# Performance work log

Hardware: AMD Instinct MI355X
Metric: run time of the kernel (lower is better)

## Reference

```python
import jax, jax.numpy as jnp
import numpy as np
import math
from jax import lax

F_SZ = 128      # feature_size
N_HEADS = 8
DH = F_SZ // N_HEADS
LANE_F = 64     # lane_feature_size
NUM_PREDS = 6
LEN_PRED = 30
B, V, T_PAST, N_LANES = 32, 64, 20, 128
SCALE = 1.0 / math.sqrt(DH)


def _heads(x):
    # [..., F] -> [..., H, dh]
    return x.reshape(*x.shape[:-1], N_HEADS, DH)


def _attn(q, k, v):
    # q: [..., H, Nq, dh], k/v: [..., H, Nk, dh] (broadcast over leading dims)
    s = jnp.einsum('...hqd,...hkd->...hqk', q, k) * SCALE
    p = jax.nn.softmax(s, axis=-1)
    return jnp.einsum('...hqk,...hkd->...hqd', p, v)


def _conv1(w, x):
    # 1x1 Conv2d (no bias): w [O,F], x [B,F,V,T]
    return jnp.einsum('of,bfvt->bovt', w, x)


def _to_tbhvd(x):
    # [B,F,V,T] -> [T,B,H,V,dh]  (matches permute(3,0,2,1).view(...).permute(0,1,3,2,4))
    return _heads(x.transpose(3, 0, 2, 1)).transpose(0, 1, 3, 2, 4)


def setup_inputs() -> dict:
    key = jax.random.key(0)
    ks = jax.random.split(key, 32)
    rn = lambda i, shp: jax.random.normal(ks[i], shp, dtype=jnp.float32)
    w = lambda i, shp: rn(i, shp) * 0.05
    return {
        'inputs': rn(0, (B, 2, V, T_PAST)),
        'lanes': rn(1, (B, N_LANES, LANE_F)),
        'pos': rn(2, (B, V, 2)),
        # Embedding conv (2 -> F, kernel (1,3), pad (0,1))
        'emb_w': w(3, (F_SZ, 2, 1, 3)), 'emb_b': w(4, (F_SZ,)),
        # LaneAttentionPast (Linear weights [out,in], no bias)
        'wq_past': w(5, (F_SZ, F_SZ)), 'wk_lanes_p': w(6, (F_SZ, LANE_F)),
        'wv_lanes_p': w(7, (F_SZ, LANE_F)), 'wc_past': w(8, (F_SZ, F_SZ)),
        # SelfAttentionFut (1x1 convs, no bias)
        'wk_fut': w(9, (F_SZ, F_SZ)), 'wq_fut_sa': w(10, (F_SZ, F_SZ)),
        'wv_fut': w(11, (F_SZ, F_SZ)), 'wc_fut_sa': w(12, (F_SZ, F_SZ)),
        # LaneAttentionFut
        'wk_lanes_f': w(13, (F_SZ, LANE_F)), 'wv_lanes_f': w(14, (F_SZ, LANE_F)),
        'wq_fut_la': w(15, (F_SZ, F_SZ)), 'wc_fut_la': w(16, (F_SZ, F_SZ)),
        # MultiOutputLayer (1x1 convs with bias)
        'w1': w(17, (F_SZ, F_SZ)), 'b1': w(18, (F_SZ,)),
        'w2': w(19, (F_SZ, F_SZ)), 'b2': w(20, (F_SZ,)),
        'wo': w(21, (6 * NUM_PREDS, F_SZ)), 'bo': w(22, (6 * NUM_PREDS,)),
    }


def reference(inputs, lanes, pos, emb_w, emb_b, wq_past, wk_lanes_p, wv_lanes_p,
              wc_past, wk_fut, wq_fut_sa, wv_fut, wc_fut_sa, wk_lanes_f,
              wv_lanes_f, wq_fut_la, wc_fut_la, w1, b1, w2, b2, wo, bo):
    # ---- Embedding: Conv2d(2->F, (1,3), pad (0,1)) over [B,2,V,T_past]
    emb = lax.conv_general_dilated(
        inputs, emb_w, (1, 1), ((0, 0), (1, 1)),
        dimension_numbers=('NCHW', 'OIHW', 'NCHW')) + emb_b[None, :, None, None]
    feat = emb[:, :, :, -1].transpose(0, 2, 1)            # [B,V,F] last timestep

    # ---- LaneAttentionPast: vehicles attend to lanes
    q = _heads(feat @ wq_past.T).transpose(0, 2, 1, 3)    # [B,H,V,dh]
    k = _heads(lanes @ wk_lanes_p.T).transpose(0, 2, 1, 3)  # [B,H,nl,dh]
    v = _heads(lanes @ wv_lanes_p.T).transpose(0, 2, 1, 3)
    o = _attn(q, k, v).transpose(0, 2, 1, 3).reshape(B, V, F_SZ)
    feat = o @ wc_past.T + feat                           # residual

    # ---- tile over prediction horizon: h [B,F,V,T]
    h = jnp.broadcast_to(feat.transpose(0, 2, 1)[:, :, :, None],
                         (B, F_SZ, V, LEN_PRED))

    # ---- SelfAttentionFut: per-timestep vehicle-vehicle attention
    k = _to_tbhvd(_conv1(wk_fut, h))                      # [T,B,H,V,dh]
    q = _to_tbhvd(_conv1(wq_fut_sa, h))
    vv = _to_tbhvd(_conv1(wv_fut, h))
    o = _attn(q, k, vv).transpose(0, 1, 3, 2, 4).reshape(LEN_PRED, B, V, F_SZ)
    h = _conv1(wc_fut_sa, o.transpose(1, 3, 2, 0)) + h    # residual

    # ---- LaneAttentionFut: per-timestep vehicle-lane attention
    kl = _heads(lanes @ wk_lanes_f.T).transpose(0, 2, 1, 3)[None]  # [1,B,H,nl,dh]
    vl = _heads(lanes @ wv_lanes_f.T).transpose(0, 2, 1, 3)[None]
    q = _to_tbhvd(_conv1(wq_fut_la, h))                   # [T,B,H,V,dh]
    o = _attn(q, kl, vl).transpose(0, 1, 3, 2, 4).reshape(LEN_PRED, B, V, F_SZ)
    h = _conv1(wc_fut_la, o.transpose(1, 3, 2, 0)) + h    # residual

    z = jax.nn.relu(_conv1(w1, h) + b1[None, :, None, None])
    z = jax.nn.relu(_conv1(w2, z) + b2[None, :, None, None])
    z = _conv1(wo, z) + bo[None, :, None, None]           # [B,6P,V,T]
    x = z.transpose(3, 0, 2, 1).reshape(LEN_PRED, B, V, NUM_PREDS, 6)

    # ---- outputActivation (Gaussian-mixture params)
    p = jax.nn.softmax(x[..., 5:6] / math.sqrt(NUM_PREDS), axis=3)
    posr = pos.reshape(1, B, V, 1, 2)
    muX = x[..., 0:1] + posr[..., 0:1]
    muY = x[..., 1:2] + posr[..., 1:2]
    sigX = jnp.exp(x[..., 2:3] * 0.5)
    sigY = jnp.exp(x[..., 3:4] * 0.5)
    rho = jnp.tanh(x[..., 4:5])
    return jnp.concatenate([muX, muY, sigX, sigY, rho, p], axis=4)
```

## Files before the change

kernel.cpp:

```cpp
#include <hip/hip_runtime.h>
#include <hip/hip_bf16.h>
#include <math.h>

typedef __hip_bfloat16 bf16;
typedef float4 f4;

#define B 32
#define V 64
#define F 128
#define NL 128
#define H 8
#define DH 16
#define LEN_PRED 30

#define WEMBW 0
#define WEMBB 768
#define WB1   896
#define WB2   1024
#define WBO   1152
#define WPOS  1192
#define WCP_T  5288
#define WCSA_T 21672
#define WCLA_T 38056
#define W1_T   54440
#define W2_T   70824
#define WO_T   87208
#define OFF_FEAT1 91904
#define OFF_FEAT2 354048
#define OFF_OSA1  616192
#define OFF_OSA2  878336

struct InPtrs { const void* p[23]; };

__device__ __forceinline__ float dot4(f4 a, f4 b) {
    return a.x * b.x + a.y * b.y + a.z * b.z + a.w * b.w;
}

__device__ __forceinline__ int detect_f32(const void* lanesraw, int t) {
    const unsigned short* u = (const unsigned short*)lanesraw;
    int lane = t & 63;
    int wild = 0;
    for (int j = 0; j < 4; j++) {
        int e = (u[lane * 4 + j] >> 7) & 0xFF;
        if (e != 0 && (e < 90 || e > 164)) wild++;
    }
    unsigned long long m = __ballot(wild > 0);
    return (__popcll(m) >= 16) ? 1 : 0;
}

__device__ __forceinline__ float ldin(const void* p, int i, int fl) {
    return fl ? ((const float*)p)[i] : __bfloat162float(((const bf16*)p)[i]);
}

__device__ __forceinline__ f4 ldin4(const void* p, int i, int fl) {
    if (fl) return *(const f4*)((const float*)p + i);
    ushort4 v = *(const ushort4*)((const unsigned short*)p + i);
    f4 r;
    r.x = __uint_as_float((unsigned)v.x << 16);
    r.y = __uint_as_float((unsigned)v.y << 16);
    r.z = __uint_as_float((unsigned)v.z << 16);
    r.w = __uint_as_float((unsigned)v.w << 16);
    return r;
}

__device__ void convert_weights(const InPtrs& ptrs, int fl, float* ws, int bid) {
    int gidx = bid * 512 + threadIdx.x;
    const int fsrc[6] = {3, 4, 18, 20, 22, 2};
    const int fsz[6]  = {768, 128, 128, 128, 36, 4096};
    const int fdst[6] = {WEMBW, WEMBB, WB1, WB2, WBO, WPOS};
    #pragma unroll
    for (int s = 0; s < 6; s++) {
        const void* src = ptrs.p[fsrc[s]];
        float* dst = ws + fdst[s];
        for (int i = gidx; i < fsz[s]; i += 131072) dst[i] = ldin(src, i, fl);
    }
    const int tsrc[6] = {8, 12, 16, 17, 19, 21};
    const int tdst[6] = {WCP_T, WCSA_T, WCLA_T, W1_T, W2_T, WO_T};
    const int tO[6]   = {128, 128, 128, 128, 128, 36};
    #pragma unroll
    for (int s = 0; s < 6; s++) {
        const void* src = ptrs.p[tsrc[s]];
        float* dst = ws + tdst[s];
        int O = tO[s], n = O * 128;
        for (int j = gidx; j < n; j += 131072) {
            int k = j / O, o = j - k * O;
            dst[j] = ldin(src, o * 128 + k, fl);
        }
    }
}

__global__ __launch_bounds__(512) void k1_lap(InPtrs ptrs, float* __restrict__ ws) {
    int bid = blockIdx.x, b = bid >> 3, h = bid & 7, t = threadIdx.x;
    int fl = detect_f32(ptrs.p[1], t);
    __shared__ __align__(16) float sm[27712];
    float* ln   = sm;
    float* xs   = sm + 8704;
    float* wql  = sm + 17152;
    float* wkl  = sm + 19264;
    float* wvl  = sm + 20352;
    float* kh   = sm + 21440;
    float* vhT  = sm + 24000;
    float* qh   = sm + 26112;
    float* rsum = sm + 27392;
    float* in4  = sm + 27456;
    float* s    = ln;
    float* osa  = ws + OFF_OSA1;

    convert_weights(ptrs, fl, ws, bid);

    {
        int lb = b * NL * 64;
        for (int i = t * 4; i < NL * 64; i += 2048) {
            f4 w = ldin4(ptrs.p[1], lb + i, fl);
            *(f4*)&ln[(i >> 6) * 68 + (i & 63)] = w;
        }
        {
            int i = t * 4;
            f4 w = ldin4(ptrs.p[5], h * 2048 + i, fl);
            *(f4*)&wql[(i >> 7) * 132 + (i & 127)] = w;
        }
        if (t < 256) {
            int i = t * 4;
            f4 w = ldin4(ptrs.p[6], h * 1024 + i, fl);
            *(f4*)&wkl[(i >> 6) * 68 + (i & 63)] = w;
            w = ldin4(ptrs.p[7], h * 1024 + i, fl);
            *(f4*)&wvl[(i >> 6) * 68 + (i & 63)] = w;
        }
        if (t < 64) {
            in4[t * 4 + 0] = ldin(ptrs.p[0], ((b * 2 + 0) * 64 + t) * 20 + 18, fl);
            in4[t * 4 + 1] = ldin(ptrs.p[0], ((b * 2 + 0) * 64 + t) * 20 + 19, fl);
            in4[t * 4 + 2] = ldin(ptrs.p[0], ((b * 2 + 1) * 64 + t) * 20 + 18, fl);
            in4[t * 4 + 3] = ldin(ptrs.p[0], ((b * 2 + 1) * 64 + t) * 20 + 19, fl);
        }
    }
    __syncthreads();
    for (int i = t; i < 8192; i += 512) {
        int v = i >> 7, c = i & 127;
        xs[v * 132 + c] = ldin(ptrs.p[4], c, fl)
            + in4[v * 4 + 0] * ldin(ptrs.p[3], c * 6 + 0, fl)
            + in4[v * 4 + 1] * ldin(ptrs.p[3], c * 6 + 1, fl)
            + in4[v * 4 + 2] * ldin(ptrs.p[3], c * 6 + 3, fl)
            + in4[v * 4 + 3] * ldin(ptrs.p[3], c * 6 + 4, fl);
    }
    __syncthreads();

    if (t < 256) {
        int l0 = t >> 3, d0 = (t & 7) * 2;
        float ak[4][2] = {}, av[4][2] = {};
        for (int kk = 0; kk < 64; kk += 4) {
            f4 L[4], WK[2], WV[2];
            #pragma unroll
            for (int m = 0; m < 4; m++) L[m] = *(const f4*)&ln[(l0 + 32 * m) * 68 + kk];
            #pragma unroll
            for (int j = 0; j < 2; j++) {
                WK[j] = *(const f4*)&wkl[(d0 + j) * 68 + kk];
                WV[j] = *(const f4*)&wvl[(d0 + j) * 68 + kk];
            }
            #pragma unroll
            for (int m = 0; m < 4; m++)
                #pragma unroll
                for (int j = 0; j < 2; j++) {
                    ak[m][j] += dot4(L[m], WK[j]);
                    av[m][j] += dot4(L[m], WV[j]);
                }
        }
        #pragma unroll
        for (int m = 0; m < 4; m++)
            #pragma unroll
            for (int j = 0; j < 2; j++) {
                int l = l0 + 32 * m, d = d0 + j;
                kh[l * 20 + d] = ak[m][j];
                vhT[d * 132 + l] = av[m][j];
            }
    } else {
        int tt = t - 256, v = tt >> 2, d0 = (tt & 3) * 4;
        float aq[4] = {};
        for (int kk = 0; kk < 128; kk += 4) {
            f4 X = *(const f4*)&xs[v * 132 + kk];
            #pragma unroll
            for (int i2 = 0; i2 < 4; i2++)
                aq[i2] += dot4(X, *(const f4*)&wql[(d0 + i2) * 132 + kk]);
        }
        #pragma unroll
        for (int i2 = 0; i2 < 4; i2++) qh[v * 20 + d0 + i2] = aq[i2];
    }
    __syncthreads();

    {
        int v0 = t >> 5, l0 = t & 31;
        float sc[4][4] = {};
        #pragma unroll
        for (int kd = 0; kd < 16; kd += 4) {
            f4 Q[4], K4[4];
            #pragma unroll
            for (int m = 0; m < 4; m++) Q[m] = *(const f4*)&qh[(v0 + 16 * m) * 20 + kd];
            #pragma unroll
            for (int i2 = 0; i2 < 4; i2++) K4[i2] = *(const f4*)&kh[(l0 + 32 * i2) * 20 + kd];
            #pragma unroll
            for (int m = 0; m < 4; m++)
                #pragma unroll
                for (int i2 = 0; i2 < 4; i2++) sc[m][i2] += dot4(Q[m], K4[i2]);
        }
        #pragma unroll
        for (int m = 0; m < 4; m++)
            #pragma unroll
            for (int i2 = 0; i2 < 4; i2++)
                s[(v0 + 16 * m) * 132 + l0 + 32 * i2] = sc[m][i2] * 0.25f;
    }
    __syncthreads();

    {
        int v = t >> 3, j = t & 7;
        float* sr = s + v * 132;
        float m = -1e30f;
        for (int k = j; k < NL; k += 8) m = fmaxf(m, sr[k]);
        for (int off = 1; off < 8; off <<= 1) m = fmaxf(m, __shfl_xor(m, off));
        float sum = 0.f;
        for (int k = j; k < NL; k += 8) { float e = __expf(sr[k] - m); sr[k] = e; sum += e; }
        for (int off = 1; off < 8; off <<= 1) sum += __shfl_xor(sum, off);
        if (j == 0) rsum[v] = sum;
    }
    __syncthreads();

    if (t < 256) {
        int v = t >> 2, d0 = (t & 3) * 4;
        float o4[4] = {};
        for (int ll = 0; ll < NL; ll += 4) {
            f4 S4 = *(const f4*)&s[v * 132 + ll];
            #pragma unroll
            for (int i2 = 0; i2 < 4; i2++)
                o4[i2] += dot4(S4, *(const f4*)&vhT[(d0 + i2) * 132 + ll]);
        }
        float* ob = osa + b * 8192 + h * 16;
        float inv = 1.0f / rsum[v];
        #pragma unroll
        for (int i2 = 0; i2 < 4; i2++) ob[v * F + d0 + i2] = o4[i2] * inv;
    }
}

__global__ __launch_bounds__(512) void k2_saf(InPtrs ptrs, float* __restrict__ ws) {
    int bid = blockIdx.x, b = bid >> 3, h = bid & 7, t = threadIdx.x;
    int fl = detect_f32(ptrs.p[1], t);
    __shared__ __align__(16) float smem[23488];
    float* osap = smem;
    float* qh   = smem;
    float* kh   = smem + 1280;
    float* vhT  = smem + 2560;
    float* s2   = smem + 3648;
    float* rsum = smem + 8000;
    float* xs   = smem + 8448;
    float* wsl  = smem + 16896;
    float* in4  = smem + 23232;

    const float* o1 = ws + OFF_OSA1 + b * 8192;
    for (int i = t * 4; i < 8192; i += 2048)
        *(f4*)&osap[(i >> 7) * 132 + (i & 127)] = *(const f4*)&o1[i];
    {
        int i = t * 4;
        f4 w = ldin4(ptrs.p[10], h * 2048 + i, fl);
        *(f4*)&wsl[(i >> 7) * 132 + (i & 127)] = w;
        w = ldin4(ptrs.p[9], h * 2048 + i, fl);
        *(f4*)&wsl[2112 + (i >> 7) * 132 + (i & 127)] = w;
        w = ldin4(ptrs.p[11], h * 2048 + i, fl);
        *(f4*)&wsl[4224 + (i >> 7) * 132 + (i & 127)] = w;
    }
    if (t < 64) {
        in4[t * 4 + 0] = ldin(ptrs.p[0], ((b * 2 + 0) * 64 + t) * 20 + 18, fl);
        in4[t * 4 + 1] = ldin(ptrs.p[0], ((b * 2 + 0) * 64 + t) * 20 + 19, fl);
        in4[t * 4 + 2] = ldin(ptrs.p[0], ((b * 2 + 1) * 64 + t) * 20 + 18, fl);
        in4[t * 4 + 3] = ldin(ptrs.p[0], ((b * 2 + 1) * 64 + t) * 20 + 19, fl);
    }
    __syncthreads();
    for (int i = t; i < 8192; i += 512) {
        int v = i >> 7, c = i & 127;
        xs[v * 132 + c] = ws[WEMBB + c]
            + in4[v * 4 + 0] * ws[WEMBW + c * 6 + 0]
            + in4[v * 4 + 1] * ws[WEMBW + c * 6 + 1]
            + in4[v * 4 + 2] * ws[WEMBW + c * 6 + 3]
            + in4[v * 4 + 3] * ws[WEMBW + c * 6 + 4];
    }
    __syncthreads();
    {
        const float* wT = ws + WCP_T;
        int v0 = (t >> 5) * 4, c0 = (t & 31) * 4;
        float acc[4][4];
        #pragma unroll
        for (int m = 0; m < 4; m++) {
            f4 X0 = *(const f4*)&xs[(v0 + m) * 132 + c0];
            acc[m][0] = X0.x; acc[m][1] = X0.y; acc[m][2] = X0.z; acc[m][3] = X0.w;
        }
        for (int k = 0; k < 128; k += 4) {
            f4 W0 = *(const f4*)&wT[(k + 0) * 128 + c0];
            f4 W1 = *(const f4*)&wT[(k + 1) * 128 + c0];
            f4 W2 = *(const f4*)&wT[(k + 2) * 128 + c0];
            f4 W3 = *(const f4*)&wT[(k + 3) * 128 + c0];
            #pragma unroll
            for (int m = 0; m < 4; m++) {
                f4 X = *(const f4*)&osap[(v0 + m) * 132 + k];
                acc[m][0] += X.x * W0.x + X.y * W1.x + X.z * W2.x + X.w * W3.x;
                acc[m][1] += X.x * W0.y + X.y * W1.y + X.z * W2.y + X.w * W3.y;
                acc[m][2] += X.x * W0.z + X.y * W1.z + X.z * W2.z + X.w * W3.z;
                acc[m][3] += X.x * W0.w + X.y * W1.w + X.z * W2.w + X.w * W3.w;
            }
        }
        #pragma unroll
        for (int m = 0; m < 4; m++)
            *(f4*)&xs[(v0 + m) * 132 + c0] =
                make_float4(acc[m][0], acc[m][1], acc[m][2], acc[m][3]);
    }
    __syncthreads();
    if (h == 0) {
        float* f1 = ws + OFF_FEAT1 + b * 8192;
        for (int i = t; i < 8192; i += 512) f1[i] = xs[(i >> 7) * 132 + (i & 127)];
    }
    __syncthreads();

    if (t < 256) {
        int v = t >> 2, d0 = (t & 3) * 4;
        float aq[4] = {};
        for (int kk = 0; kk < 128; kk += 4) {
            f4 X = *(const f4*)&xs[v * 132 + kk];
            #pragma unroll
            for (int i2 = 0; i2 < 4; i2++)
                aq[i2] += dot4(X, *(const f4*)&wsl[(d0 + i2) * 132 + kk]);
        }
        #pragma unroll
        for (int i2 = 0; i2 < 4; i2++) qh[v * 20 + d0 + i2] = aq[i2];
    } else if (t < 384) {
        int tt = t - 256, v = tt >> 1, d0 = (tt & 1) * 8;
        float ak[8] = {};
        for (int kk = 0; kk < 128; kk += 4) {
            f4 X = *(const f4*)&xs[v * 132 + kk];
            #pragma unroll
            for (int i2 = 0; i2 < 8; i2++)
                ak[i2] += dot4(X, *(const f4*)&wsl[2112 + (d0 + i2) * 132 + kk]);
        }
        #pragma unroll
        for (int i2 = 0; i2 < 8; i2++) kh[v * 20 + d0 + i2] = ak[i2];
    } else {
        int tt = t - 384, v = tt >> 1, d0 = (tt & 1) * 8;
        float av[8] = {};
        for (int kk = 0; kk < 128; kk += 4) {
            f4 X = *(const f4*)&xs[v * 132 + kk];
            #pragma unroll
            for (int i2 = 0; i2 < 8; i2++)
                av[i2] += dot4(X, *(const f4*)&wsl[4224 + (d0 + i2) * 132 + kk]);
        }
        #pragma unroll
        for (int i2 = 0; i2 < 8; i2++) vhT[(d0 + i2) * 68 + v] = av[i2];
    }
    __syncthreads();

    {
        int v0 = t >> 5, l0 = t & 31;
        float sc[4][2] = {};
        #pragma unroll
        for (int kd = 0; kd < 16; kd += 4) {
            f4 Q[4], K2[2];
            #pragma unroll
            for (int m = 0; m < 4; m++) Q[m] = *(const f4*)&qh[(v0 + 16 * m) * 20 + kd];
            #pragma unroll
            for (int i2 = 0; i2 < 2; i2++) K2[i2] = *(const f4*)&kh[(l0 + 32 * i2) * 20 + kd];
            #pragma unroll
            for (int m = 0; m < 4; m++)
                #pragma unroll
                for (int i2 = 0; i2 < 2; i2++) sc[m][i2] += dot4(Q[m], K2[i2]);
        }
        #pragma unroll
        for (int m = 0; m < 4; m++)
            #pragma unroll
            for (int i2 = 0; i2 < 2; i2++)
                s2[(v0 + 16 * m) * 68 + l0 + 32 * i2] = sc[m][i2] * 0.25f;
    }
    __syncthreads();

    {
        int v = t >> 3, j = t & 7;
        float* sr = s2 + v * 68;
        float m = -1e30f;
        for (int k = j; k < V; k += 8) m = fmaxf(m, sr[k]);
        for (int off = 1; off < 8; off <<= 1) m = fmaxf(m, __shfl_xor(m, off));
        float sum = 0.f;
        for (int k = j; k < V; k += 8) { float e = __expf(sr[k] - m); sr[k] = e; sum += e; }
        for (int off = 1; off < 8; off <<= 1) sum += __shfl_xor(sum, off);
        if (j == 0) rsum[v] = sum;
    }
    __syncthreads();

    if (t < 256) {
        int v = t >> 2, d0 = (t & 3) * 4;
        float o4[4] = {};
        for (int ll = 0; ll < V; ll += 4) {
            f4 S4 = *(const f4*)&s2[v * 68 + ll];
            #pragma unroll
            for (int i2 = 0; i2 < 4; i2++)
                o4[i2] += dot4(S4, *(const f4*)&vhT[(d0 + i2) * 68 + ll]);
        }
        float* ob = ws + OFF_OSA2 + b * 8192 + h * 16;
        float inv = 1.0f / rsum[v];
        #pragma unroll
        for (int i2 = 0; i2 < 4; i2++) ob[v * F + d0 + i2] = o4[i2] * inv;
    }
}

__global__ __launch_bounds__(512) void k3_laf(InPtrs ptrs, float* __restrict__ ws) {
    int bid = blockIdx.x, b = bid >> 3, h = bid & 7, t = threadIdx.x;
    int fl = detect_f32(ptrs.p[1], t);
    __shared__ __align__(16) float smem[29888];
    float* ln   = smem;
    float* osas = smem + 8704;
    float* kh   = smem + 8704;
    float* vhT  = smem + 11264;
    float* qh   = smem + 13376;
    float* rsum = smem + 14656;
    float* xs   = smem + 17152;
    float* wql  = smem + 25600;
    float* wkl  = smem + 27712;
    float* wvl  = smem + 28800;
    float* s    = ln;

    {
        int lb = b * NL * 64;
        for (int i = t * 4; i < NL * 64; i += 2048) {
            f4 w = ldin4(ptrs.p[1], lb + i, fl);
            *(f4*)&ln[(i >> 6) * 68 + (i & 63)] = w;
        }
        const float* o2 = ws + OFF_OSA2 + b * 8192;
        for (int i = t * 4; i < 8192; i += 2048)
            *(f4*)&osas[(i >> 7) * 132 + (i & 127)] = *(const f4*)&o2[i];
        {
            int i = t * 4;
            f4 w = ldin4(ptrs.p[15], h * 2048 + i, fl);
            *(f4*)&wql[(i >> 7) * 132 + (i & 127)] = w;
        }
        if (t < 256) {
            int i = t * 4;
            f4 w = ldin4(ptrs.p[13], h * 1024 + i, fl);
            *(f4*)&wkl[(i >> 6) * 68 + (i & 63)] = w;
            w = ldin4(ptrs.p[14], h * 1024 + i, fl);
            *(f4*)&wvl[(i >> 6) * 68 + (i & 63)] = w;
        }
    }
    __syncthreads();
    {
        const float* wT = ws + WCSA_T;
        const float* f1 = ws + OFF_FEAT1 + b * 8192;
        int v0 = (t >> 5) * 4, c0 = (t & 31) * 4;
        float acc[4][4];
        #pragma unroll
        for (int m = 0; m < 4; m++) {
            f4 X0 = *(const f4*)&f1[(v0 + m) * 128 + c0];
            acc[m][0] = X0.x; acc[m][1] = X0.y; acc[m][2] = X0.z; acc[m][3] = X0.w;
        }
        for (int k = 0; k < 128; k += 4) {
            f4 W0 = *(const f4*)&wT[(k + 0) * 128 + c0];
            f4 W1 = *(const f4*)&wT[(k + 1) * 128 + c0];
            f4 W2 = *(const f4*)&wT[(k + 2) * 128 + c0];
            f4 W3 = *(const f4*)&wT[(k + 3) * 128 + c0];
            #pragma unroll
            for (int m = 0; m < 4; m++) {
                f4 X = *(const f4*)&osas[(v0 + m) * 132 + k];
                acc[m][0] += X.x * W0.x + X.y * W1.x + X.z * W2.x + X.w * W3.x;
                acc[m][1] += X.x * W0.y + X.y * W1.y + X.z * W2.y + X.w * W3.y;
                acc[m][2] += X.x * W0.z + X.y * W1.z + X.z * W2.z + X.w * W3.z;
                acc[m][3] += X.x * W0.w + X.y * W1.w + X.z * W2.w + X.w * W3.w;
            }
        }
        #pragma unroll
        for (int m = 0; m < 4; m++)
            *(f4*)&xs[(v0 + m) * 132 + c0] =
                make_float4(acc[m][0], acc[m][1], acc[m][2], acc[m][3]);
    }
    __syncthreads();
    if (h == 0) {
        float* f2 = ws + OFF_FEAT2 + b * 8192;
        for (int i = t; i < 8192; i += 512) f2[i] = xs[(i >> 7) * 132 + (i & 127)];
    }
    __syncthreads();

    if (t < 256) {
        int l0 = t >> 3, d0 = (t & 7) * 2;
        float ak[4][2] = {}, av[4][2] = {};
        for (int kk = 0; kk < 64; kk += 4) {
            f4 L[4], WK[2], WV[2];
            #pragma unroll
            for (int m = 0; m < 4; m++) L[m] = *(const f4*)&ln[(l0 + 32 * m) * 68 + kk];
            #pragma unroll
            for (int j = 0; j < 2; j++) {
                WK[j] = *(const f4*)&wkl[(d0 + j) * 68 + kk];
                WV[j] = *(const f4*)&wvl[(d0 + j) * 68 + kk];
            }
            #pragma unroll
            for (int m = 0; m < 4; m++)
                #pragma unroll
                for (int j = 0; j < 2; j++) {
                    ak[m][j] += dot4(L[m], WK[j]);
                    av[m][j] += dot4(L[m], WV[j]);
                }
        }
        #pragma unroll
        for (int m = 0; m < 4; m++)
            #pragma unroll
            for (int j = 0; j < 2; j++) {
                int l = l0 + 32 * m, d = d0 + j;
                kh[l * 20 + d] = ak[m][j];
                vhT[d * 132 + l] = av[m][j];
            }
    } else {
        int tt = t - 256, v = tt >> 2, d0 = (tt & 3) * 4;
        float aq[4] = {};
        for (int kk = 0; kk < 128; kk += 4) {
            f4 X = *(const f4*)&xs[v * 132 + kk];
            #pragma unroll
            for (int i2 = 0; i2 < 4; i2++)
                aq[i2] += dot4(X, *(const f4*)&wql[(d0 + i2) * 132 + kk]);
        }
        #pragma unroll
        for (int i2 = 0; i2 < 4; i2++) qh[v * 20 + d0 + i2] = aq[i2];
    }
    __syncthreads();

    {
        int v0 = t >> 5, l0 = t & 31;
        float sc[4][4] = {};
        #pragma unroll
        for (int kd = 0; kd < 16; kd += 4) {
            f4 Q[4], K4[4];
            #pragma unroll
            for (int m = 0; m < 4; m++) Q[m] = *(const f4*)&qh[(v0 + 16 * m) * 20 + kd];
            #pragma unroll
            for (int i2 = 0; i2 < 4; i2++) K4[i2] = *(const f4*)&kh[(l0 + 32 * i2) * 20 + kd];
            #pragma unroll
            for (int m = 0; m < 4; m++)
                #pragma unroll
                for (int i2 = 0; i2 < 4; i2++) sc[m][i2] += dot4(Q[m], K4[i2]);
        }
        #pragma unroll
        for (int m = 0; m < 4; m++)
            #pragma unroll
            for (int i2 = 0; i2 < 4; i2++)
                s[(v0 + 16 * m) * 132 + l0 + 32 * i2] = sc[m][i2] * 0.25f;
    }
    __syncthreads();

    {
        int v = t >> 3, j = t & 7;
        float* sr = s + v * 132;
        float m = -1e30f;
        for (int k = j; k < NL; k += 8) m = fmaxf(m, sr[k]);
        for (int off = 1; off < 8; off <<= 1) m = fmaxf(m, __shfl_xor(m, off));
        float sum = 0.f;
        for (int k = j; k < NL; k += 8) { float e = __expf(sr[k] - m); sr[k] = e; sum += e; }
        for (int off = 1; off < 8; off <<= 1) sum += __shfl_xor(sum, off);
        if (j == 0) rsum[v] = sum;
    }
    __syncthreads();

    if (t < 256) {
        int v = t >> 2, d0 = (t & 3) * 4;
        float o4[4] = {};
        for (int ll = 0; ll < NL; ll += 4) {
            f4 S4 = *(const f4*)&s[v * 132 + ll];
            #pragma unroll
            for (int i2 = 0; i2 < 4; i2++)
                o4[i2] += dot4(S4, *(const f4*)&vhT[(d0 + i2) * 132 + ll]);
        }
        float* ob = ws + OFF_OSA1 + b * 8192 + h * 16;
        float inv = 1.0f / rsum[v];
        #pragma unroll
        for (int i2 = 0; i2 < 4; i2++) ob[v * F + d0 + i2] = o4[i2] * inv;
    }
}

__global__ __launch_bounds__(512) void k4_out(InPtrs ptrs, float* __restrict__ ws,
                                              void* __restrict__ out) {
    int bid = blockIdx.x, t = threadIdx.x;
    int fl = detect_f32(ptrs.p[1], t);
    __shared__ __align__(16) float sm[4416];
    const float* ola  = ws + OFF_OSA1;
    const float* feat = ws + OFF_FEAT2;
    int bvl = t >> 6, u = t & 63;
    int bv = bid * 8 + bvl;
    float* orow = sm + bvl * 128;
    float* h3   = sm + 1024 + bvl * 128;
    float* z1   = sm + 2048 + bvl * 128;
    float* z2   = sm + 3072 + bvl * 128;
    float* z3all = sm + 4096;
    float* z3   = z3all + bvl * 40;
    orow[u] = ola[bv * 128 + u];
    orow[u + 64] = ola[bv * 128 + u + 64];
    __syncthreads();
    const float* wclaT = ws + WCLA_T;
    float a0 = 0.f, a1 = 0.f;
    for (int k = 0; k < 128; k++) {
        float x = orow[k];
        a0 += x * wclaT[k * 128 + u]; a1 += x * wclaT[k * 128 + u + 64];
    }
    h3[u] = a0 + feat[bv * 128 + u];
    h3[u + 64] = a1 + feat[bv * 128 + u + 64];
    __syncthreads();
    const float* w1T = ws + W1_T;
    a0 = ws[WB1 + u]; a1 = ws[WB1 + u + 64];
    for (int k = 0; k < 128; k++) {
        float x = h3[k];
        a0 += x * w1T[k * 128 + u]; a1 += x * w1T[k * 128 + u + 64];
    }
    z1[u] = fmaxf(a0, 0.f); z1[u + 64] = fmaxf(a1, 0.f);
    __syncthreads();
    const float* w2T = ws + W2_T;
    a0 = ws[WB2 + u]; a1 = ws[WB2 + u + 64];
    for (int k = 0; k < 128; k++) {
        float x = z1[k];
        a0 += x * w2T[k * 128 + u]; a1 += x * w2T[k * 128 + u + 64];
    }
    z2[u] = fmaxf(a0, 0.f); z2[u + 64] = fmaxf(a1, 0.f);
    __syncthreads();
    const float* woT = ws + WO_T;
    if (u < 36) {
        float a = ws[WBO + u];
        for (int k = 0; k < 128; k++) a += z2[k] * woT[k * 36 + u];
        z3[u] = a;
    }
    __syncthreads();
    float r = 0.f;
    if (u < 36) {
        int c = u % 6;
        float xv = z3[u];
        if (c == 0)      r = xv + ws[WPOS + bv * 2 + 0];
        else if (c == 1) r = xv + ws[WPOS + bv * 2 + 1];
        else if (c == 2 || c == 3) r = __expf(0.5f * xv);
        else if (c == 4) r = tanhf(xv);
        else {
            const float inv = 0.4082482904638631f;
            float m = -1e30f;
            for (int pp = 0; pp < 6; pp++) m = fmaxf(m, z3[pp * 6 + 5] * inv);
            float sum = 0.f;
            for (int pp = 0; pp < 6; pp++) sum += __expf(z3[pp * 6 + 5] * inv - m);
            r = __expf(xv * inv - m) / sum;
        }
    }
    __syncthreads();
    if (u < 36) z3[u] = r;
    __syncthreads();
    int base = bid * 288;
    if (fl) {
        float* o = (float*)out;
        for (int i = t; i < LEN_PRED * 288; i += 512) {
            int ttp = i / 288, idx = i - ttp * 288;
            o[ttp * 73728 + base + idx] = z3all[(idx / 36) * 40 + idx % 36];
        }
    } else {
        bf16* o = (bf16*)out;
        for (int i = t; i < LEN_PRED * 288; i += 512) {
            int ttp = i / 288, idx = i - ttp * 288;
            o[ttp * 73728 + base + idx] = __float2bfloat16(z3all[(idx / 36) * 40 + idx % 36]);
        }
    }
}

extern "C" void kernel_launch(void* const* d_in, const int* in_sizes, int n_in,
                              void* d_out, int out_size, void* d_ws, size_t ws_size,
                              hipStream_t stream) {
    float* ws = (float*)d_ws;
    InPtrs ptrs;
    for (int i = 0; i < 23; i++) ptrs.p[i] = d_in[i];
    k1_lap<<<256, 512, 0, stream>>>(ptrs, ws);
    k2_saf<<<256, 512, 0, stream>>>(ptrs, ws);
    k3_laf<<<256, 512, 0, stream>>>(ptrs, ws);
    k4_out<<<256, 512, 0, stream>>>(ptrs, ws, d_out);
}
```

Baseline: 100.3 us.

## Double threads per block to 1024 and halve per-thread work in all kernels

All four kernels launch with 1024 threads instead of 512. Every phase (projections, score GEMMs, softmax, PV, MLP) is remapped so each thread computes half as many outputs, and the weight-loading work is split across thread ranges. The aim is more parallelism per block and lower per-thread latency on a grid of only 256 blocks. In exchange each thread does less register-level reuse, there are more redundant shared-memory loads, and barriers cover larger blocks.

```diff
diff --git a/kernel.cpp b/kernel.cpp
--- a/kernel.cpp
+++ b/kernel.cpp
@@ -64,7 +64,7 @@
 }
 
 __device__ void convert_weights(const InPtrs& ptrs, int fl, float* ws, int bid) {
-    int gidx = bid * 512 + threadIdx.x;
+    int gidx = bid * 1024 + threadIdx.x;
     const int fsrc[6] = {3, 4, 18, 20, 22, 2};
     const int fsz[6]  = {768, 128, 128, 128, 36, 4096};
     const int fdst[6] = {WEMBW, WEMBB, WB1, WB2, WBO, WPOS};
@@ -72,7 +72,7 @@
     for (int s = 0; s < 6; s++) {
         const void* src = ptrs.p[fsrc[s]];
         float* dst = ws + fdst[s];
-        for (int i = gidx; i < fsz[s]; i += 131072) dst[i] = ldin(src, i, fl);
+        for (int i = gidx; i < fsz[s]; i += 262144) dst[i] = ldin(src, i, fl);
     }
     const int tsrc[6] = {8, 12, 16, 17, 19, 21};
     const int tdst[6] = {WCP_T, WCSA_T, WCLA_T, W1_T, W2_T, WO_T};
@@ -82,14 +82,14 @@
         const void* src = ptrs.p[tsrc[s]];
         float* dst = ws + tdst[s];
         int O = tO[s], n = O * 128;
-        for (int j = gidx; j < n; j += 131072) {
+        for (int j = gidx; j < n; j += 262144) {
             int k = j / O, o = j - k * O;
             dst[j] = ldin(src, o * 128 + k, fl);
         }
     }
 }
 
-__global__ __launch_bounds__(512) void k1_lap(InPtrs ptrs, float* __restrict__ ws) {
+__global__ __launch_bounds__(1024) void k1_lap(InPtrs ptrs, float* __restrict__ ws) {
     int bid = blockIdx.x, b = bid >> 3, h = bid & 7, t = threadIdx.x;
     int fl = detect_f32(ptrs.p[1], t);
     __shared__ __align__(16) float sm[27712];
@@ -110,20 +110,21 @@
 
     {
         int lb = b * NL * 64;
-        for (int i = t * 4; i < NL * 64; i += 2048) {
+        for (int i = t * 4; i < NL * 64; i += 4096) {
             f4 w = ldin4(ptrs.p[1], lb + i, fl);
             *(f4*)&ln[(i >> 6) * 68 + (i & 63)] = w;
         }
-        {
+        if (t < 512) {
             int i = t * 4;
             f4 w = ldin4(ptrs.p[5], h * 2048 + i, fl);
             *(f4*)&wql[(i >> 7) * 132 + (i & 127)] = w;
-        }
-        if (t < 256) {
-            int i = t * 4;
+        } else if (t < 768) {
+            int i = (t - 512) * 4;
             f4 w = ldin4(ptrs.p[6], h * 1024 + i, fl);
             *(f4*)&wkl[(i >> 6) * 68 + (i & 63)] = w;
-            w = ldin4(ptrs.p[7], h * 1024 + i, fl);
+        } else {
+            int i = (t - 768) * 4;
+            f4 w = ldin4(ptrs.p[7], h * 1024 + i, fl);
             *(f4*)&wvl[(i >> 6) * 68 + (i & 63)] = w;
         }
         if (t < 64) {
@@ -134,7 +135,7 @@
         }
     }
     __syncthreads();
-    for (int i = t; i < 8192; i += 512) {
+    for (int i = t; i < 8192; i += 1024) {
         int v = i >> 7, c = i & 127;
         xs[v * 132 + c] = ldin(ptrs.p[4], c, fl)
             + in4[v * 4 + 0] * ldin(ptrs.p[3], c * 6 + 0, fl)
@@ -144,20 +145,20 @@
     }
     __syncthreads();
 
-    if (t < 256) {
-        int l0 = t >> 3, d0 = (t & 7) * 2;
-        float ak[4][2] = {}, av[4][2] = {};
+    if (t < 512) {
+        int l0 = t & 63, d0 = (t >> 6) * 2;
+        float ak[2][2] = {}, av[2][2] = {};
         for (int kk = 0; kk < 64; kk += 4) {
-            f4 L[4], WK[2], WV[2];
-            #pragma unroll
-            for (int m = 0; m < 4; m++) L[m] = *(const f4*)&ln[(l0 + 32 * m) * 68 + kk];
+            f4 L[2], WK[2], WV[2];
+            #pragma unroll
+            for (int m = 0; m < 2; m++) L[m] = *(const f4*)&ln[(l0 + 64 * m) * 68 + kk];
             #pragma unroll
             for (int j = 0; j < 2; j++) {
                 WK[j] = *(const f4*)&wkl[(d0 + j) * 68 + kk];
                 WV[j] = *(const f4*)&wvl[(d0 + j) * 68 + kk];
             }
             #pragma unroll
-            for (int m = 0; m < 4; m++)
+            for (int m = 0; m < 2; m++)
                 #pragma unroll
                 for (int j = 0; j < 2; j++) {
                     ak[m][j] += dot4(L[m], WK[j]);
@@ -165,80 +166,80 @@
                 }
         }
         #pragma unroll
-        for (int m = 0; m < 4; m++)
+        for (int m = 0; m < 2; m++)
             #pragma unroll
             for (int j = 0; j < 2; j++) {
-                int l = l0 + 32 * m, d = d0 + j;
+                int l = l0 + 64 * m, d = d0 + j;
                 kh[l * 20 + d] = ak[m][j];
                 vhT[d * 132 + l] = av[m][j];
             }
     } else {
-        int tt = t - 256, v = tt >> 2, d0 = (tt & 3) * 4;
-        float aq[4] = {};
+        int tt = t - 512, v = tt >> 3, d0 = (tt & 7) * 2;
+        float aq[2] = {};
         for (int kk = 0; kk < 128; kk += 4) {
             f4 X = *(const f4*)&xs[v * 132 + kk];
             #pragma unroll
-            for (int i2 = 0; i2 < 4; i2++)
-                aq[i2] += dot4(X, *(const f4*)&wql[(d0 + i2) * 132 + kk]);
-        }
-        #pragma unroll
-        for (int i2 = 0; i2 < 4; i2++) qh[v * 20 + d0 + i2] = aq[i2];
-    }
-    __syncthreads();
-
-    {
-        int v0 = t >> 5, l0 = t & 31;
-        float sc[4][4] = {};
+            for (int j = 0; j < 2; j++)
+                aq[j] += dot4(X, *(const f4*)&wql[(d0 + j) * 132 + kk]);
+        }
+        #pragma unroll
+        for (int j = 0; j < 2; j++) qh[v * 20 + d0 + j] = aq[j];
+    }
+    __syncthreads();
+
+    {
+        int v0 = t >> 6, l0 = t & 63;
+        float sc[4][2] = {};
         #pragma unroll
         for (int kd = 0; kd < 16; kd += 4) {
-            f4 Q[4], K4[4];
+            f4 Q[4], K2[2];
             #pragma unroll
             for (int m = 0; m < 4; m++) Q[m] = *(const f4*)&qh[(v0 + 16 * m) * 20 + kd];
             #pragma unroll
-            for (int i2 = 0; i2 < 4; i2++) K4[i2] = *(const f4*)&kh[(l0 + 32 * i2) * 20 + kd];
+            for (int i2 = 0; i2 < 2; i2++) K2[i2] = *(const f4*)&kh[(l0 + 64 * i2) * 20 + kd];
             #pragma unroll
             for (int m = 0; m < 4; m++)
                 #pragma unroll
-                for (int i2 = 0; i2 < 4; i2++) sc[m][i2] += dot4(Q[m], K4[i2]);
+                for (int i2 = 0; i2 < 2; i2++) sc[m][i2] += dot4(Q[m], K2[i2]);
         }
         #pragma unroll
         for (int m = 0; m < 4; m++)
             #pragma unroll
-            for (int i2 = 0; i2 < 4; i2++)
-                s[(v0 + 16 * m) * 132 + l0 + 32 * i2] = sc[m][i2] * 0.25f;
-    }
-    __syncthreads();
-
-    {
-        int v = t >> 3, j = t & 7;
+            for (int i2 = 0; i2 < 2; i2++)
+                s[(v0 + 16 * m) * 132 + l0 + 64 * i2] = sc[m][i2] * 0.25f;
+    }
+    __syncthreads();
+
+    {
+        int v = t >> 4, j = t & 15;
         float* sr = s + v * 132;
         float m = -1e30f;
-        for (int k = j; k < NL; k += 8) m = fmaxf(m, sr[k]);
-        for (int off = 1; off < 8; off <<= 1) m = fmaxf(m, __shfl_xor(m, off));
+        for (int k = j; k < NL; k += 16) m = fmaxf(m, sr[k]);
+        for (int off = 1; off < 16; off <<= 1) m = fmaxf(m, __shfl_xor(m, off));
         float sum = 0.f;
-        for (int k = j; k < NL; k += 8) { float e = __expf(sr[k] - m); sr[k] = e; sum += e; }
-        for (int off = 1; off < 8; off <<= 1) sum += __shfl_xor(sum, off);
+        for (int k = j; k < NL; k += 16) { float e = __expf(sr[k] - m); sr[k] = e; sum += e; }
+        for (int off = 1; off < 16; off <<= 1) sum += __shfl_xor(sum, off);
         if (j == 0) rsum[v] = sum;
     }
     __syncthreads();
 
-    if (t < 256) {
-        int v = t >> 2, d0 = (t & 3) * 4;
-        float o4[4] = {};
+    if (t < 512) {
+        int v = t >> 3, d0 = (t & 7) * 2;
+        float o2[2] = {};
         for (int ll = 0; ll < NL; ll += 4) {
             f4 S4 = *(const f4*)&s[v * 132 + ll];
             #pragma unroll
-            for (int i2 = 0; i2 < 4; i2++)
-                o4[i2] += dot4(S4, *(const f4*)&vhT[(d0 + i2) * 132 + ll]);
+            for (int j = 0; j < 2; j++)
+                o2[j] += dot4(S4, *(const f4*)&vhT[(d0 + j) * 132 + ll]);
         }
         float* ob = osa + b * 8192 + h * 16;
         float inv = 1.0f / rsum[v];
         #pragma unroll
-        for (int i2 = 0; i2 < 4; i2++) ob[v * F + d0 + i2] = o4[i2] * inv;
-    }
-}
-
-__global__ __launch_bounds__(512) void k2_saf(InPtrs ptrs, float* __restrict__ ws) {
+        for (int j = 0; j < 2; j++) ob[v * F + d0 + j] = o2[j] * inv;
+    }
+}
+
+__global__ __launch_bounds__(1024) void k2_saf(InPtrs ptrs, float* __restrict__ ws) {
     int bid = blockIdx.x, b = bid >> 3, h = bid & 7, t = threadIdx.x;
     int fl = detect_f32(ptrs.p[1], t);
     __shared__ __align__(16) float smem[23488];
@@ -253,16 +254,16 @@
     float* in4  = smem + 23232;
 
     const float* o1 = ws + OFF_OSA1 + b * 8192;
-    for (int i = t * 4; i < 8192; i += 2048)
+    for (int i = t * 4; i < 8192; i += 4096)
         *(f4*)&osap[(i >> 7) * 132 + (i & 127)] = *(const f4*)&o1[i];
     {
-        int i = t * 4;
-        f4 w = ldin4(ptrs.p[10], h * 2048 + i, fl);
-        *(f4*)&wsl[(i >> 7) * 132 + (i & 127)] = w;
-        w = ldin4(ptrs.p[9], h * 2048 + i, fl);
-        *(f4*)&wsl[2112 + (i >> 7) * 132 + (i & 127)] = w;
-        w = ldin4(ptrs.p[11], h * 2048 + i, fl);
-        *(f4*)&wsl[4224 + (i >> 7) * 132 + (i & 127)] = w;
+        int i = (t & 511) * 4;
+        if (t < 512) {
+            *(f4*)&wsl[(i >> 7) * 132 + (i & 127)] = ldin4(ptrs.p[10], h * 2048 + i, fl);
+            *(f4*)&wsl[4224 + (i >> 7) * 132 + (i & 127)] = ldin4(ptrs.p[11], h * 2048 + i, fl);
+        } else {
+            *(f4*)&wsl[2112 + (i >> 7) * 132 + (i & 127)] = ldin4(ptrs.p[9], h * 2048 + i, fl);
+        }
     }
     if (t < 64) {
         in4[t * 4 + 0] = ldin(ptrs.p[0], ((b * 2 + 0) * 64 + t) * 20 + 18, fl);
@@ -271,7 +272,7 @@
         in4[t * 4 + 3] = ldin(ptrs.p[0], ((b * 2 + 1) * 64 + t) * 20 + 19, fl);
     }
     __syncthreads();
-    for (int i = t; i < 8192; i += 512) {
+    for (int i = t; i < 8192; i += 1024) {
         int v = i >> 7, c = i & 127;
         xs[v * 132 + c] = ws[WEMBB + c]
             + in4[v * 4 + 0] * ws[WEMBW + c * 6 + 0]
@@ -282,10 +283,10 @@
     __syncthreads();
     {
         const float* wT = ws + WCP_T;
-        int v0 = (t >> 5) * 4, c0 = (t & 31) * 4;
-        float acc[4][4];
-        #pragma unroll
-        for (int m = 0; m < 4; m++) {
+        int v0 = (t >> 5) * 2, c0 = (t & 31) * 4;
+        float acc[2][4];
+        #pragma unroll
+        for (int m = 0; m < 2; m++) {
             f4 X0 = *(const f4*)&xs[(v0 + m) * 132 + c0];
             acc[m][0] = X0.x; acc[m][1] = X0.y; acc[m][2] = X0.z; acc[m][3] = X0.w;
         }
@@ -295,7 +296,7 @@
             f4 W2 = *(const f4*)&wT[(k + 2) * 128 + c0];
             f4 W3 = *(const f4*)&wT[(k + 3) * 128 + c0];
             #pragma unroll
-            for (int m = 0; m < 4; m++) {
+            for (int m = 0; m < 2; m++) {
                 f4 X = *(const f4*)&osap[(v0 + m) * 132 + k];
                 acc[m][0] += X.x * W0.x + X.y * W1.x + X.z * W2.x + X.w * W3.x;
                 acc[m][1] += X.x * W0.y + X.y * W1.y + X.z * W2.y + X.w * W3.y;
@@ -304,106 +305,95 @@
             }
         }
         #pragma unroll
-        for (int m = 0; m < 4; m++)
+        for (int m = 0; m < 2; m++)
             *(f4*)&xs[(v0 + m) * 132 + c0] =
                 make_float4(acc[m][0], acc[m][1], acc[m][2], acc[m][3]);
     }
     __syncthreads();
     if (h == 0) {
         float* f1 = ws + OFF_FEAT1 + b * 8192;
-        for (int i = t; i < 8192; i += 512) f1[i] = xs[(i >> 7) * 132 + (i & 127)];
-    }
-    __syncthreads();
-
-    if (t < 256) {
-        int v = t >> 2, d0 = (t & 3) * 4;
-        float aq[4] = {};
+        for (int i = t; i < 8192; i += 1024) f1[i] = xs[(i >> 7) * 132 + (i & 127)];
+    }
+    __syncthreads();
+
+    if (t < 512) {
+        int v = t >> 3, d0 = (t & 7) * 2;
+        float aq[2] = {};
         for (int kk = 0; kk < 128; kk += 4) {
             f4 X = *(const f4*)&xs[v * 132 + kk];
             #pragma unroll
-            for (int i2 = 0; i2 < 4; i2++)
-                aq[i2] += dot4(X, *(const f4*)&wsl[(d0 + i2) * 132 + kk]);
-        }
-        #pragma unroll
-        for (int i2 = 0; i2 < 4; i2++) qh[v * 20 + d0 + i2] = aq[i2];
-    } else if (t < 384) {
-        int tt = t - 256, v = tt >> 1, d0 = (tt & 1) * 8;
-        float ak[8] = {};
+            for (int j = 0; j < 2; j++)
+                aq[j] += dot4(X, *(const f4*)&wsl[(d0 + j) * 132 + kk]);
+        }
+        #pragma unroll
+        for (int j = 0; j < 2; j++) qh[v * 20 + d0 + j] = aq[j];
+    } else if (t < 768) {
+        int tt = t - 512, v = tt >> 2, d0 = (tt & 3) * 4;
+        float ak[4] = {};
         for (int kk = 0; kk < 128; kk += 4) {
             f4 X = *(const f4*)&xs[v * 132 + kk];
             #pragma unroll
-            for (int i2 = 0; i2 < 8; i2++)
-                ak[i2] += dot4(X, *(const f4*)&wsl[2112 + (d0 + i2) * 132 + kk]);
-        }
-        #pragma unroll
-        for (int i2 = 0; i2 < 8; i2++) kh[v * 20 + d0 + i2] = ak[i2];
+            for (int j = 0; j < 4; j++)
+                ak[j] += dot4(X, *(const f4*)&wsl[2112 + (d0 + j) * 132 + kk]);
+        }
+        #pragma unroll
+        for (int j = 0; j < 4; j++) kh[v * 20 + d0 + j] = ak[j];
     } else {
-        int tt = t - 384, v = tt >> 1, d0 = (tt & 1) * 8;
-        float av[8] = {};
+        int tt = t - 768, v = tt >> 2, d0 = (tt & 3) * 4;
+        float av[4] = {};
         for (int kk = 0; kk < 128; kk += 4) {
             f4 X = *(const f4*)&xs[v * 132 + kk];
             #pragma unroll
-            for (int i2 = 0; i2 < 8; i2++)
-                av[i2] += dot4(X, *(const f4*)&wsl[4224 + (d0 + i2) * 132 + kk]);
-        }
-        #pragma unroll
-        for (int i2 = 0; i2 < 8; i2++) vhT[(d0 + i2) * 68 + v] = av[i2];
-    }
-    __syncthreads();
-
-    {
-        int v0 = t >> 5, l0 = t & 31;
-        float sc[4][2] = {};
+            for (int j = 0; j < 4; j++)
+                av[j] += dot4(X, *(const f4*)&wsl[4224 + (d0 + j) * 132 + kk]);
+        }
+        #pragma unroll
+        for (int j = 0; j < 4; j++) vhT[(d0 + j) * 68 + v] = av[j];
+    }
+    __syncthreads();
+
+    {
+        int v0 = t >> 6, l = t & 63;
+        float sc[4] = {};
         #pragma unroll
         for (int kd = 0; kd < 16; kd += 4) {
-            f4 Q[4], K2[2];
-            #pragma unroll
-            for (int m = 0; m < 4; m++) Q[m] = *(const f4*)&qh[(v0 + 16 * m) * 20 + kd];
-            #pragma unroll
-            for (int i2 = 0; i2 < 2; i2++) K2[i2] = *(const f4*)&kh[(l0 + 32 * i2) * 20 + kd];
+            f4 Kr = *(const f4*)&kh[l * 20 + kd];
             #pragma unroll
             for (int m = 0; m < 4; m++)
-                #pragma unroll
-                for (int i2 = 0; i2 < 2; i2++) sc[m][i2] += dot4(Q[m], K2[i2]);
+                sc[m] += dot4(*(const f4*)&qh[(v0 + 16 * m) * 20 + kd], Kr);
         }
         #pragma unroll
         for (int m = 0; m < 4; m++)
-            #pragma unroll
-            for (int i2 = 0; i2 < 2; i2++)
-                s2[(v0 + 16 * m) * 68 + l0 + 32 * i2] = sc[m][i2] * 0.25f;
-    }
-    __syncthreads();
-
-    {
-        int v = t >> 3, j = t & 7;
+            s2[(v0 + 16 * m) * 68 + l] = sc[m] * 0.25f;
+    }
+    __syncthreads();
+
+    {
+        int v = t >> 4, j = t & 15;
         float* sr = s2 + v * 68;
         float m = -1e30f;
-        for (int k = j; k < V; k += 8) m = fmaxf(m, sr[k]);
-        for (int off = 1; off < 8; off <<= 1) m = fmaxf(m, __shfl_xor(m, off));
+        for (int k = j; k < V; k += 16) m = fmaxf(m, sr[k]);
+        for (int off = 1; off < 16; off <<= 1) m = fmaxf(m, __shfl_xor(m, off));
         float sum = 0.f;
-        for (int k = j; k < V; k += 8) { float e = __expf(sr[k] - m); sr[k] = e; sum += e; }
-        for (int off = 1; off < 8; off <<= 1) sum += __shfl_xor(sum, off);
+        for (int k = j; k < V; k += 16) { float e = __expf(sr[k] - m); sr[k] = e; sum += e; }
+        for (int off = 1; off < 16; off <<= 1) sum += __shfl_xor(sum, off);
         if (j == 0) rsum[v] = sum;
     }
     __syncthreads();
 
-    if (t < 256) {
-        int v = t >> 2, d0 = (t & 3) * 4;
-        float o4[4] = {};
+    {
+        int v = t >> 4, d = t & 15;
+        float o = 0.f;
         for (int ll = 0; ll < V; ll += 4) {
             f4 S4 = *(const f4*)&s2[v * 68 + ll];
-            #pragma unroll
-            for (int i2 = 0; i2 < 4; i2++)
-                o4[i2] += dot4(S4, *(const f4*)&vhT[(d0 + i2) * 68 + ll]);
+            o += dot4(S4, *(const f4*)&vhT[d * 68 + ll]);
         }
         float* ob = ws + OFF_OSA2 + b * 8192 + h * 16;
-        float inv = 1.0f / rsum[v];
-        #pragma unroll
-        for (int i2 = 0; i2 < 4; i2++) ob[v * F + d0 + i2] = o4[i2] * inv;
-    }
-}
-
-__global__ __launch_bounds__(512) void k3_laf(InPtrs ptrs, float* __restrict__ ws) {
+        ob[v * F + d] = o / rsum[v];
+    }
+}
+
+__global__ __launch_bounds__(1024) void k3_laf(InPtrs ptrs, float* __restrict__ ws) {
     int bid = blockIdx.x, b = bid >> 3, h = bid & 7, t = threadIdx.x;
     int fl = detect_f32(ptrs.p[1], t);
     __shared__ __align__(16) float smem[29888];
@@ -421,23 +411,24 @@
 
     {
         int lb = b * NL * 64;
-        for (int i = t * 4; i < NL * 64; i += 2048) {
+        for (int i = t * 4; i < NL * 64; i += 4096) {
             f4 w = ldin4(ptrs.p[1], lb + i, fl);
             *(f4*)&ln[(i >> 6) * 68 + (i & 63)] = w;
         }
         const float* o2 = ws + OFF_OSA2 + b * 8192;
-        for (int i = t * 4; i < 8192; i += 2048)
+        for (int i = t * 4; i < 8192; i += 4096)
             *(f4*)&osas[(i >> 7) * 132 + (i & 127)] = *(const f4*)&o2[i];
-        {
+        if (t < 512) {
             int i = t * 4;
             f4 w = ldin4(ptrs.p[15], h * 2048 + i, fl);
             *(f4*)&wql[(i >> 7) * 132 + (i & 127)] = w;
-        }
-        if (t < 256) {
-            int i = t * 4;
+        } else if (t < 768) {
+            int i = (t - 512) * 4;
             f4 w = ldin4(ptrs.p[13], h * 1024 + i, fl);
             *(f4*)&wkl[(i >> 6) * 68 + (i & 63)] = w;
-            w = ldin4(ptrs.p[14], h * 1024 + i, fl);
+        } else {
+            int i = (t - 768) * 4;
+            f4 w = ldin4(ptrs.p[14], h * 1024 + i, fl);
             *(f4*)&wvl[(i >> 6) * 68 + (i & 63)] = w;
         }
     }
@@ -445,10 +436,10 @@
     {
         const float* wT = ws + WCSA_T;
         const float* f1 = ws + OFF_FEAT1 + b * 8192;
-        int v0 = (t >> 5) * 4, c0 = (t & 31) * 4;
-        float acc[4][4];
-        #pragma unroll
-        for (int m = 0; m < 4; m++) {
+        int v0 = (t >> 5) * 2, c0 = (t & 31) * 4;
+        float acc[2][4];
+        #pragma unroll
+        for (int m = 0; m < 2; m++) {
             f4 X0 = *(const f4*)&f1[(v0 + m) * 128 + c0];
             acc[m][0] = X0.x; acc[m][1] = X0.y; acc[m][2] = X0.z; acc[m][3] = X0.w;
         }
@@ -458,7 +449,7 @@
             f4 W2 = *(const f4*)&wT[(k + 2) * 128 + c0];
             f4 W3 = *(const f4*)&wT[(k + 3) * 128 + c0];
             #pragma unroll
-            for (int m = 0; m < 4; m++) {
+            for (int m = 0; m < 2; m++) {
                 f4 X = *(const f4*)&osas[(v0 + m) * 132 + k];
                 acc[m][0] += X.x * W0.x + X.y * W1.x + X.z * W2.x + X.w * W3.x;
                 acc[m][1] += X.x * W0.y + X.y * W1.y + X.z * W2.y + X.w * W3.y;
@@ -467,31 +458,31 @@
             }
         }
         #pragma unroll
-        for (int m = 0; m < 4; m++)
+        for (int m = 0; m < 2; m++)
             *(f4*)&xs[(v0 + m) * 132 + c0] =
                 make_float4(acc[m][0], acc[m][1], acc[m][2], acc[m][3]);
     }
     __syncthreads();
     if (h == 0) {
         float* f2 = ws + OFF_FEAT2 + b * 8192;
-        for (int i = t; i < 8192; i += 512) f2[i] = xs[(i >> 7) * 132 + (i & 127)];
-    }
-    __syncthreads();
-
-    if (t < 256) {
-        int l0 = t >> 3, d0 = (t & 7) * 2;
-        float ak[4][2] = {}, av[4][2] = {};
+        for (int i = t; i < 8192; i += 1024) f2[i] = xs[(i >> 7) * 132 + (i & 127)];
+    }
+    __syncthreads();
+
+    if (t < 512) {
+        int l0 = t & 63, d0 = (t >> 6) * 2;
+        float ak[2][2] = {}, av[2][2] = {};
         for (int kk = 0; kk < 64; kk += 4) {
-            f4 L[4], WK[2], WV[2];
-            #pragma unroll
-            for (int m = 0; m < 4; m++) L[m] = *(const f4*)&ln[(l0 + 32 * m) * 68 + kk];
+            f4 L[2], WK[2], WV[2];
+            #pragma unroll
+            for (int m = 0; m < 2; m++) L[m] = *(const f4*)&ln[(l0 + 64 * m) * 68 + kk];
             #pragma unroll
             for (int j = 0; j < 2; j++) {
                 WK[j] = *(const f4*)&wkl[(d0 + j) * 68 + kk];
                 WV[j] = *(const f4*)&wvl[(d0 + j) * 68 + kk];
             }
             #pragma unroll
-            for (int m = 0; m < 4; m++)
+            for (int m = 0; m < 2; m++)
                 #pragma unroll
                 for (int j = 0; j < 2; j++) {
                     ak[m][j] += dot4(L[m], WK[j]);
@@ -499,87 +490,87 @@
                 }
         }
         #pragma unroll
-        for (int m = 0; m < 4; m++)
+        for (int m = 0; m < 2; m++)
             #pragma unroll
             for (int j = 0; j < 2; j++) {
-                int l = l0 + 32 * m, d = d0 + j;
+                int l = l0 + 64 * m, d = d0 + j;
                 kh[l * 20 + d] = ak[m][j];
                 vhT[d * 132 + l] = av[m][j];
             }
     } else {
-        int tt = t - 256, v = tt >> 2, d0 = (tt & 3) * 4;
-        float aq[4] = {};
+        int tt = t - 512, v = tt >> 3, d0 = (tt & 7) * 2;
+        float aq[2] = {};
         for (int kk = 0; kk < 128; kk += 4) {
             f4 X = *(const f4*)&xs[v * 132 + kk];
             #pragma unroll
-            for (int i2 = 0; i2 < 4; i2++)
-                aq[i2] += dot4(X, *(const f4*)&wql[(d0 + i2) * 132 + kk]);
-        }
-        #pragma unroll
-        for (int i2 = 0; i2 < 4; i2++) qh[v * 20 + d0 + i2] = aq[i2];
-    }
-    __syncthreads();
-
-    {
-        int v0 = t >> 5, l0 = t & 31;
-        float sc[4][4] = {};
+            for (int j = 0; j < 2; j++)
+                aq[j] += dot4(X, *(const f4*)&wql[(d0 + j) * 132 + kk]);
+        }
+        #pragma unroll
+        for (int j = 0; j < 2; j++) qh[v * 20 + d0 + j] = aq[j];
+    }
+    __syncthreads();
+
+    {
+        int v0 = t >> 6, l0 = t & 63;
+        float sc[4][2] = {};
         #pragma unroll
         for (int kd = 0; kd < 16; kd += 4) {
-            f4 Q[4], K4[4];
+            f4 Q[4], K2[2];
             #pragma unroll
             for (int m = 0; m < 4; m++) Q[m] = *(const f4*)&qh[(v0 + 16 * m) * 20 + kd];
             #pragma unroll
-            for (int i2 = 0; i2 < 4; i2++) K4[i2] = *(const f4*)&kh[(l0 + 32 * i2) * 20 + kd];
+            for (int i2 = 0; i2 < 2; i2++) K2[i2] = *(const f4*)&kh[(l0 + 64 * i2) * 20 + kd];
             #pragma unroll
             for (int m = 0; m < 4; m++)
                 #pragma unroll
-                for (int i2 = 0; i2 < 4; i2++) sc[m][i2] += dot4(Q[m], K4[i2]);
+                for (int i2 = 0; i2 < 2; i2++) sc[m][i2] += dot4(Q[m], K2[i2]);
         }
         #pragma unroll
         for (int m = 0; m < 4; m++)
             #pragma unroll
-            for (int i2 = 0; i2 < 4; i2++)
-                s[(v0 + 16 * m) * 132 + l0 + 32 * i2] = sc[m][i2] * 0.25f;
-    }
-    __syncthreads();
-
-    {
-        int v = t >> 3, j = t & 7;
+            for (int i2 = 0; i2 < 2; i2++)
+                s[(v0 + 16 * m) * 132 + l0 + 64 * i2] = sc[m][i2] * 0.25f;
+    }
+    __syncthreads();
+
+    {
+        int v = t >> 4, j = t & 15;
         float* sr = s + v * 132;
         float m = -1e30f;
-        for (int k = j; k < NL; k += 8) m = fmaxf(m, sr[k]);
-        for (int off = 1; off < 8; off <<= 1) m = fmaxf(m, __shfl_xor(m, off));
+        for (int k = j; k < NL; k += 16) m = fmaxf(m, sr[k]);
+        for (int off = 1; off < 16; off <<= 1) m = fmaxf(m, __shfl_xor(m, off));
         float sum = 0.f;
-        for (int k = j; k < NL; k += 8) { float e = __expf(sr[k] - m); sr[k] = e; sum += e; }
-        for (int off = 1; off < 8; off <<= 1) sum += __shfl_xor(sum, off);
+        for (int k = j; k < NL; k += 16) { float e = __expf(sr[k] - m); sr[k] = e; sum += e; }
+        for (int off = 1; off < 16; off <<= 1) sum += __shfl_xor(sum, off);
         if (j == 0) rsum[v] = sum;
     }
     __syncthreads();
 
-    if (t < 256) {
-        int v = t >> 2, d0 = (t & 3) * 4;
-        float o4[4] = {};
+    if (t < 512) {
+        int v = t >> 3, d0 = (t & 7) * 2;
+        float o2[2] = {};
         for (int ll = 0; ll < NL; ll += 4) {
             f4 S4 = *(const f4*)&s[v * 132 + ll];
             #pragma unroll
-            for (int i2 = 0; i2 < 4; i2++)
-                o4[i2] += dot4(S4, *(const f4*)&vhT[(d0 + i2) * 132 + ll]);
+            for (int j = 0; j < 2; j++)
+                o2[j] += dot4(S4, *(const f4*)&vhT[(d0 + j) * 132 + ll]);
         }
         float* ob = ws + OFF_OSA1 + b * 8192 + h * 16;
         float inv = 1.0f / rsum[v];
         #pragma unroll
-        for (int i2 = 0; i2 < 4; i2++) ob[v * F + d0 + i2] = o4[i2] * inv;
-    }
-}
-
-__global__ __launch_bounds__(512) void k4_out(InPtrs ptrs, float* __restrict__ ws,
-                                              void* __restrict__ out) {
+        for (int j = 0; j < 2; j++) ob[v * F + d0 + j] = o2[j] * inv;
+    }
+}
+
+__global__ __launch_bounds__(1024) void k4_out(InPtrs ptrs, float* __restrict__ ws,
+                                               void* __restrict__ out) {
     int bid = blockIdx.x, t = threadIdx.x;
     int fl = detect_f32(ptrs.p[1], t);
     __shared__ __align__(16) float sm[4416];
     const float* ola  = ws + OFF_OSA1;
     const float* feat = ws + OFF_FEAT2;
-    int bvl = t >> 6, u = t & 63;
+    int bvl = t >> 7, u = t & 127;
     int bv = bid * 8 + bvl;
     float* orow = sm + bvl * 128;
     float* h3   = sm + 1024 + bvl * 128;
@@ -588,32 +579,21 @@
     float* z3all = sm + 4096;
     float* z3   = z3all + bvl * 40;
     orow[u] = ola[bv * 128 + u];
-    orow[u + 64] = ola[bv * 128 + u + 64];
     __syncthreads();
     const float* wclaT = ws + WCLA_T;
-    float a0 = 0.f, a1 = 0.f;
-    for (int k = 0; k < 128; k++) {
-        float x = orow[k];
-        a0 += x * wclaT[k * 128 + u]; a1 += x * wclaT[k * 128 + u + 64];
-    }
+    float a0 = 0.f;
+    for (int k = 0; k < 128; k++) a0 += orow[k] * wclaT[k * 128 + u];
     h3[u] = a0 + feat[bv * 128 + u];
-    h3[u + 64] = a1 + feat[bv * 128 + u + 64];
     __syncthreads();
     const float* w1T = ws + W1_T;
-    a0 = ws[WB1 + u]; a1 = ws[WB1 + u + 64];
-    for (int k = 0; k < 128; k++) {
-        float x = h3[k];
-        a0 += x * w1T[k * 128 + u]; a1 += x * w1T[k * 128 + u + 64];
-    }
-    z1[u] = fmaxf(a0, 0.f); z1[u + 64] = fmaxf(a1, 0.f);
+    a0 = ws[WB1 + u];
+    for (int k = 0; k < 128; k++) a0 += h3[k] * w1T[k * 128 + u];
+    z1[u] = fmaxf(a0, 0.f);
     __syncthreads();
     const float* w2T = ws + W2_T;
-    a0 = ws[WB2 + u]; a1 = ws[WB2 + u + 64];
-    for (int k = 0; k < 128; k++) {
-        float x = z1[k];
-        a0 += x * w2T[k * 128 + u]; a1 += x * w2T[k * 128 + u + 64];
-    }
-    z2[u] = fmaxf(a0, 0.f); z2[u + 64] = fmaxf(a1, 0.f);
+    a0 = ws[WB2 + u];
+    for (int k = 0; k < 128; k++) a0 += z1[k] * w2T[k * 128 + u];
+    z2[u] = fmaxf(a0, 0.f);
     __syncthreads();
     const float* woT = ws + WO_T;
     if (u < 36) {
@@ -645,13 +625,13 @@
     int base = bid * 288;
     if (fl) {
         float* o = (float*)out;
-        for (int i = t; i < LEN_PRED * 288; i += 512) {
+        for (int i = t; i < LEN_PRED * 288; i += 1024) {
             int ttp = i / 288, idx = i - ttp * 288;
             o[ttp * 73728 + base + idx] = z3all[(idx / 36) * 40 + idx % 36];
         }
     } else {
         bf16* o = (bf16*)out;
-        for (int i = t; i < LEN_PRED * 288; i += 512) {
+        for (int i = t; i < LEN_PRED * 288; i += 1024) {
             int ttp = i / 288, idx = i - ttp * 288;
             o[ttp * 73728 + base + idx] = __float2bfloat16(z3all[(idx / 36) * 40 + idx % 36]);
         }
@@ -664,8 +644,8 @@
     float* ws = (float*)d_ws;
     InPtrs ptrs;
     for (int i = 0; i < 23; i++) ptrs.p[i] = d_in[i];
-    k1_lap<<<256, 512, 0, stream>>>(ptrs, ws);
-    k2_saf<<<256, 512, 0, stream>>>(ptrs, ws);
-    k3_laf<<<256, 512, 0, stream>>>(ptrs, ws);
-    k4_out<<<256, 512, 0, stream>>>(ptrs, ws, d_out);
-}
+    k1_lap<<<256, 1024, 0, stream>>>(ptrs, ws);
+    k2_saf<<<256, 1024, 0, stream>>>(ptrs, ws);
+    k3_laf<<<256, 1024, 0, stream>>>(ptrs, ws);
+    k4_out<<<256, 1024, 0, stream>>>(ptrs, ws, d_out);
+}
```

Measured after the change: 105.1 us. 1.05x slower.
